# Kernel optimization log

Measured on AMD Instinct MI355X. Metric: run time of the kernel, lower is better.

Reference implementation:

```python
import jax, jax.numpy as jnp
import numpy as np

E = 1024      # hidden_size
H = 16        # num_attention_heads
HD = E // H   # head_dim
EPS = 1e-5


def _mw_linear(x, Wt, bt, Wi, bi, split):
    # multiway linear: text weights on tokens [:split], image weights on [split:]
    xt = x[:, :split] @ Wt.T + bt
    xi = x[:, split:] @ Wi.T + bi
    return jnp.concatenate([xt, xi], axis=1)


def _ln(x, g, b):
    mu = jnp.mean(x, axis=-1, keepdims=True)
    var = jnp.mean(jnp.square(x - mu), axis=-1, keepdims=True)
    return (x - mu) * jax.lax.rsqrt(var + EPS) * g + b


def _mw_ln(x, gt, bt, gi, bi, split):
    return jnp.concatenate([_ln(x[:, :split], gt, bt), _ln(x[:, split:], gi, bi)], axis=1)


def setup_inputs() -> dict:
    key = jax.random.key(0)
    ks = jax.random.split(key, 24)
    B, T = 8, 1024
    d = {
        'query': jax.random.normal(ks[0], (B, T, E), jnp.float32),
        'key': jax.random.normal(ks[1], (B, T, E), jnp.float32),
        'value': jax.random.normal(ks[2], (B, T, E), jnp.float32),
        'attention_mask': jax.random.normal(ks[3], (T, T), jnp.float32) * 0.02,
    }
    i = 4
    for name in ['q', 'k', 'v', 'o']:
        d[f'W{name}_t'] = jax.random.normal(ks[i], (E, E), jnp.float32) * 0.02; i += 1
        d[f'b{name}_t'] = jnp.zeros((E,), jnp.float32)
        d[f'W{name}_i'] = jax.random.normal(ks[i], (E, E), jnp.float32) * 0.02; i += 1
        d[f'b{name}_i'] = jnp.zeros((E,), jnp.float32)
    d['ln_g_t'] = jnp.ones((E,), jnp.float32)
    d['ln_b_t'] = jnp.zeros((E,), jnp.float32)
    d['ln_g_i'] = jnp.ones((E,), jnp.float32)
    d['ln_b_i'] = jnp.zeros((E,), jnp.float32)
    d['split_position'] = 64
    return d


def reference(query, key, value, attention_mask,
              Wq_t, bq_t, Wq_i, bq_i,
              Wk_t, bk_t, Wk_i, bk_i,
              Wv_t, bv_t, Wv_i, bv_i,
              Wo_t, bo_t, Wo_i, bo_i,
              ln_g_t, ln_b_t, ln_g_i, ln_b_i,
              split_position):
    B, T, _ = query.shape
    S = key.shape[1]
    scaling = HD ** -0.5
    q = _mw_linear(query, Wq_t, bq_t, Wq_i, bq_i, split_position) * scaling
    k = _mw_linear(key, Wk_t, bk_t, Wk_i, bk_i, split_position)
    v = _mw_linear(value, Wv_t, bv_t, Wv_i, bv_i, split_position)
    q = q.reshape(B, T, H, HD)
    k = k.reshape(B, S, H, HD)
    v = v.reshape(B, S, H, HD)
    # [B, H, T, S] attention logits
    attn_weights = jnp.einsum('bthd,bshd->bhts', q, k)
    attn_weights = jnp.nan_to_num(attn_weights) + attention_mask[None, None]
    probs = jax.nn.softmax(attn_weights.astype(jnp.float32), axis=-1).astype(attn_weights.dtype)
    attn = jnp.einsum('bhts,bshd->bthd', probs, v).reshape(B, T, E)
    attn = _mw_ln(attn, ln_g_t, ln_b_t, ln_g_i, ln_b_i, split_position)
    attn = _mw_linear(attn, Wo_t, bo_t, Wo_i, bo_i, split_position)
    return attn
```

## Files before the change

### kernel.cpp

```cpp
#include <hip/hip_runtime.h>

#define E_DIM 1024
#define HEADS 16
#define HD 64

typedef unsigned short ushort_t;
typedef __attribute__((ext_vector_type(8))) short bf16x8;
typedef __attribute__((ext_vector_type(4))) float floatx4;

__device__ inline unsigned int pack2bf(float a, float b) {
    unsigned int ua = __builtin_bit_cast(unsigned int, a);
    unsigned int ub = __builtin_bit_cast(unsigned int, b);
    ua = (ua + 0x8000u) >> 16;
    ub = (ub + 0x8000u) & 0xFFFF0000u;
    return ua | ub;
}
__device__ inline unsigned short f2bf(float a) {
    return (unsigned short)((__builtin_bit_cast(unsigned int, a) + 0x8000u) >> 16);
}
__device__ inline float bf2f(unsigned int s) {
    return __builtin_bit_cast(float, s << 16);
}

__device__ __forceinline__ void load_lds16(const void* g, void* l) {
    __builtin_amdgcn_global_load_lds(
        (const __attribute__((address_space(1))) unsigned int*)g,
        (__attribute__((address_space(3))) unsigned int*)l, 16, 0, 0);
}

__global__ __launch_bounds__(256) void cvt_inputs(
    const float* s0, const float* s1, const float* s2,
    ushort_t* d0, ushort_t* d1, ushort_t* d2)
{
    const float* __restrict__ src = (blockIdx.y == 0) ? s0 : (blockIdx.y == 1) ? s1 : s2;
    ushort_t* __restrict__ dst = (blockIdx.y == 0) ? d0 : (blockIdx.y == 1) ? d1 : d2;
    size_t i = ((size_t)blockIdx.x * 256 + threadIdx.x) * 8;
    float4 a = *(const float4*)&src[i];
    float4 b = *(const float4*)&src[i + 4];
    uint4 o;
    o.x = pack2bf(a.x, a.y); o.y = pack2bf(a.z, a.w);
    o.z = pack2bf(b.x, b.y); o.w = pack2bf(b.z, b.w);
    *(uint4*)&dst[i] = o;
}

__global__ __launch_bounds__(256) void cvt_weights(
    const float* w0, const float* w1, const float* w2, const float* w3,
    const float* w4, const float* w5, const float* w6, const float* w7,
    ushort_t* __restrict__ out)
{
    const float* srcs[8] = {w0, w1, w2, w3, w4, w5, w6, w7};
    const float* __restrict__ src = srcs[blockIdx.y];
    ushort_t* __restrict__ dst = out + (size_t)blockIdx.y * E_DIM * E_DIM;
    size_t i = ((size_t)blockIdx.x * 256 + threadIdx.x) * 8;
    float4 a = *(const float4*)&src[i];
    float4 b = *(const float4*)&src[i + 4];
    uint4 o;
    o.x = pack2bf(a.x, a.y); o.y = pack2bf(a.z, a.w);
    o.z = pack2bf(b.x, b.y); o.w = pack2bf(b.z, b.w);
    *(uint4*)&dst[i] = o;
}

template<bool OUT_BF16>
__device__ __forceinline__ void gemm_core(
    const ushort_t* __restrict__ x, const ushort_t* __restrict__ W,
    const float* __restrict__ bias, void* __restrict__ outv,
    int m0, int n0, int split, int kind, float scale, int T_)
{
    __shared__ __align__(16) ushort_t As[128 * 32];
    __shared__ __align__(16) ushort_t Bs[128 * 32];

    const int tid  = threadIdx.x;
    const int lane = tid & 63;
    const int wv   = tid >> 6;
    const int rw   = (wv >> 1) * 64;
    const int cw   = (wv & 1) * 64;
    const int am   = lane & 15;
    const int aq   = lane >> 4;

    const int grow = wv * 32 + (lane >> 2);
    const int gcol = (lane & 3) * 8;

    floatx4 acc[4][4];
    #pragma unroll
    for (int i = 0; i < 4; ++i)
        #pragma unroll
        for (int j = 0; j < 4; ++j)
            acc[i][j] = (floatx4){0.f, 0.f, 0.f, 0.f};

    for (int k0 = 0; k0 < E_DIM; k0 += 32) {
        load_lds16(&x[(size_t)(m0 + grow) * E_DIM + k0 + gcol],      &As[(wv * 32) * 32]);
        load_lds16(&x[(size_t)(m0 + grow + 16) * E_DIM + k0 + gcol], &As[(wv * 32 + 16) * 32]);
        load_lds16(&W[(size_t)(n0 + grow) * E_DIM + k0 + gcol],      &Bs[(wv * 32) * 32]);
        load_lds16(&W[(size_t)(n0 + grow + 16) * E_DIM + k0 + gcol], &Bs[(wv * 32 + 16) * 32]);
        __syncthreads();

        bf16x8 af[4], bfv[4];
        #pragma unroll
        for (int i = 0; i < 4; ++i)
            af[i] = *(const bf16x8*)&As[(rw + i * 16 + am) * 32 + aq * 8];
        #pragma unroll
        for (int j = 0; j < 4; ++j)
            bfv[j] = *(const bf16x8*)&Bs[(cw + j * 16 + am) * 32 + aq * 8];

        #pragma unroll
        for (int i = 0; i < 4; ++i)
            #pragma unroll
            for (int j = 0; j < 4; ++j)
                acc[i][j] = __builtin_amdgcn_mfma_f32_16x16x32_bf16(af[i], bfv[j], acc[i][j], 0, 0, 0);
        __syncthreads();
    }

    const int cq = lane >> 4;
    const int cm = lane & 15;
    #pragma unroll
    for (int j = 0; j < 4; ++j) {
        int n = n0 + cw + j * 16 + cm;
        float bv = bias[n];
        #pragma unroll
        for (int i = 0; i < 4; ++i) {
            int mbase = m0 + rw + i * 16 + cq * 4;
            #pragma unroll
            for (int r = 0; r < 4; ++r) {
                int m = mbase + r;
                int t = m % T_;
                if (((t < split) ? 0 : 1) != kind) continue;
                float val = (acc[i][j][r] + bv) * scale;
                if (OUT_BF16) ((ushort_t*)outv)[(size_t)m * E_DIM + n] = f2bf(val);
                else          ((float*)outv)[(size_t)m * E_DIM + n] = val;
            }
        }
    }
}

__global__ __launch_bounds__(256) void gemm_qkv(
    const ushort_t* __restrict__ xq, const ushort_t* __restrict__ xk,
    const ushort_t* __restrict__ xv, const ushort_t* __restrict__ wall,
    const float* bq_t, const float* bq_i, const float* bk_t, const float* bk_i,
    const float* bv_t, const float* bv_i,
    ushort_t* oq, ushort_t* ok, ushort_t* ov,
    const int* __restrict__ split_ptr, int T_)
{
    const int split = *split_ptr;
    const int z = blockIdx.z;
    const int op = z >> 1;
    const int kind = z & 1;
    const int m0 = blockIdx.y * 128;
    const int n0 = blockIdx.x * 128;
    const int t0 = m0 % T_;

    if (kind == 0) { if (t0 >= split) return; }
    else           { if (t0 + 128 <= split) return; }

    const ushort_t* x = (op == 0) ? xq : (op == 1) ? xk : xv;
    ushort_t* outp    = (op == 0) ? oq : (op == 1) ? ok : ov;
    const ushort_t* W = wall + (size_t)z * E_DIM * E_DIM;
    const float* bias = (op == 0) ? (kind ? bq_i : bq_t)
                      : (op == 1) ? (kind ? bk_i : bk_t)
                                  : (kind ? bv_i : bv_t);
    float scale = (op == 0) ? 0.125f : 1.0f;

    gemm_core<true>(x, W, bias, outp, m0, n0, split, kind, scale, T_);
}

__global__ __launch_bounds__(256) void gemm_o(
    const ushort_t* __restrict__ x, const ushort_t* __restrict__ Wt,
    const float* bt, const ushort_t* __restrict__ Wi, const float* bi,
    float* __restrict__ outp, const int* __restrict__ split_ptr, int T_)
{
    const int split = *split_ptr;
    const int kind = blockIdx.z;
    const int m0 = blockIdx.y * 128;
    const int n0 = blockIdx.x * 128;
    const int t0 = m0 % T_;

    if (kind == 0) { if (t0 >= split) return; }
    else           { if (t0 + 128 <= split) return; }

    gemm_core<false>(x, kind ? Wi : Wt, kind ? bi : bt, outp, m0, n0, split, kind, 1.0f, T_);
}

__global__ __launch_bounds__(256) void attn_mfma4(
    const ushort_t* __restrict__ q, const ushort_t* __restrict__ k,
    const ushort_t* __restrict__ v, const float* __restrict__ mask,
    ushort_t* __restrict__ outp, int T_)
{
    const int tid  = threadIdx.x;
    const int lane = tid & 63;
    const int wv   = tid >> 6;
    const int h    = blockIdx.y;
    const int b    = blockIdx.z;
    const int r0   = blockIdx.x * 128;

    __shared__ __align__(16) unsigned short Ks[2 * 5120];
    __shared__ __align__(16) unsigned short Vst[2 * 5120];
    __shared__ __align__(16) unsigned short Ps[4 * 1280];

    const int m    = lane & 15;
    const int kq   = lane >> 4;
    const int wrow = wv * 16;

    bf16x8 aq[2][2];
    #pragma unroll
    for (int qs = 0; qs < 2; ++qs)
        #pragma unroll
        for (int c = 0; c < 2; ++c)
            aq[qs][c] = *(const bf16x8*)&q[((size_t)(b * T_ + r0 + qs * 64 + wrow + m)) * E_DIM
                                           + h * HD + c * 32 + kq * 8];

    floatx4 oa[2][4];
    float mrun[2][4], lsum[2][4];
    #pragma unroll
    for (int qs = 0; qs < 2; ++qs)
        #pragma unroll
        for (int j = 0; j < 4; ++j) {
            oa[qs][j] = (floatx4){0.f, 0.f, 0.f, 0.f};
            mrun[qs][j] = -3.0e38f; lsum[qs][j] = 0.f;
        }

    const int krow = tid >> 4;
    const int kc4  = (tid & 15) * 4;
    const int kad  = (kc4 >> 5) * 2560 + krow * 40 + (kc4 & 31);
    const int vs0  = (tid >> 4) * 4;
    const int vd0  = (tid & 15) * 4;
    const int vplane = (vs0 >> 5) * 2560;
    const int vsin   = vs0 & 31;

    uint2 kreg[4], vreg[4];

    #pragma unroll
    for (int i = 0; i < 4; ++i)
        kreg[i] = *(const uint2*)&k[((size_t)(b * T_ + krow + 16 * i)) * E_DIM + h * HD + kc4];
    #pragma unroll
    for (int i = 0; i < 4; ++i)
        vreg[i] = *(const uint2*)&v[((size_t)(b * T_ + vs0 + i)) * E_DIM + h * HD + vd0];

    #pragma unroll
    for (int i = 0; i < 4; ++i) {
        int ad = kad + 16 * i * 40;
        *(unsigned int*)&Ks[ad]     = kreg[i].x;
        *(unsigned int*)&Ks[ad + 2] = kreg[i].y;
    }
    {
        const ushort_t* vp = (const ushort_t*)vreg;
        #pragma unroll
        for (int t = 0; t < 4; ++t) {
            int d  = vd0 + t;
            int pr = d ^ ((d >> 4) & 3);
            uint2 w;
            w.x = (unsigned int)vp[0 * 4 + t] | ((unsigned int)vp[1 * 4 + t] << 16);
            w.y = (unsigned int)vp[2 * 4 + t] | ((unsigned int)vp[3 * 4 + t] << 16);
            *(uint2*)&Vst[vplane + pr * 40 + vsin] = w;
        }
    }
    __syncthreads();

    const int NT = T_ / 64;
    #pragma unroll 1
    for (int it = 0; it < NT; ++it) {
        const int cur = (it & 1) * 5120;
        const int nxt = ((it + 1) & 1) * 5120;
        const int s0 = it * 64;

        if (it + 1 < NT) {
            int s0n = s0 + 64;
            #pragma unroll
            for (int i = 0; i < 4; ++i)
                kreg[i] = *(const uint2*)&k[((size_t)(b * T_ + s0n + krow + 16 * i)) * E_DIM + h * HD + kc4];
            #pragma unroll
            for (int i = 0; i < 4; ++i)
                vreg[i] = *(const uint2*)&v[((size_t)(b * T_ + s0n + vs0 + i)) * E_DIM + h * HD + vd0];
        }

        #pragma unroll
        for (int qs = 0; qs < 2; ++qs) {
            float mv[4][4];
            {
                const float* mbase = &mask[(size_t)(r0 + qs * 64 + wrow + kq * 4) * T_ + s0 + m];
                #pragma unroll
                for (int j = 0; j < 4; ++j)
                    #pragma unroll
                    for (int r = 0; r < 4; ++r)
                        mv[j][r] = mbase[r * T_ + j * 16];
            }

            floatx4 sa[4];
            #pragma unroll
            for (int j = 0; j < 4; ++j) sa[j] = (floatx4){0.f, 0.f, 0.f, 0.f};
            #pragma unroll
            for (int c = 0; c < 2; ++c) {
                #pragma unroll
                for (int j = 0; j < 4; ++j) {
                    bf16x8 bk = *(const bf16x8*)&Ks[cur + c * 2560 + (j * 16 + m) * 40 + kq * 8];
                    sa[j] = __builtin_amdgcn_mfma_f32_16x16x32_bf16(aq[qs][c], bk, sa[j], 0, 0, 0);
                }
            }

            float mnew[4], alpha[4];
            #pragma unroll
            for (int r = 0; r < 4; ++r) {
                sa[0][r] += mv[0][r]; sa[1][r] += mv[1][r];
                sa[2][r] += mv[2][r]; sa[3][r] += mv[3][r];
                float mt = fmaxf(fmaxf(sa[0][r], sa[1][r]), fmaxf(sa[2][r], sa[3][r]));
                mt = fmaxf(mt, __shfl_xor(mt, 1));
                mt = fmaxf(mt, __shfl_xor(mt, 2));
                mt = fmaxf(mt, __shfl_xor(mt, 4));
                mt = fmaxf(mt, __shfl_xor(mt, 8));
                float mn = fmaxf(mrun[qs][r], mt);
                alpha[r] = __expf(mrun[qs][r] - mn);
                mnew[r] = mn;
                mrun[qs][r] = mn;
            }
            #pragma unroll
            for (int j = 0; j < 4; ++j)
                #pragma unroll
                for (int r = 0; r < 4; ++r)
                    oa[qs][j][r] *= alpha[r];

            float rs[4] = {0.f, 0.f, 0.f, 0.f};
            #pragma unroll
            for (int j = 0; j < 4; ++j) {
                int gl = ((((j & 1) << 1) | (m >> 3)) ^ kq) & 3;
                int pbase = wv * 1280 + (j >> 1) * 640 + (kq * 4) * 40 + gl * 8 + (m & 7);
                #pragma unroll
                for (int r = 0; r < 4; ++r) {
                    float p = __expf(sa[j][r] - mnew[r]);
                    rs[r] += p;
                    Ps[pbase + r * 40] = f2bf(p);
                }
            }
            #pragma unroll
            for (int r = 0; r < 4; ++r) {
                float s = rs[r];
                s += __shfl_xor(s, 1); s += __shfl_xor(s, 2);
                s += __shfl_xor(s, 4); s += __shfl_xor(s, 8);
                lsum[qs][r] = lsum[qs][r] * alpha[r] + s;
            }

            #pragma unroll
            for (int c = 0; c < 2; ++c) {
                bf16x8 ap = *(const bf16x8*)&Ps[wv * 1280 + c * 640 + m * 40 + ((kq ^ (m >> 2)) & 3) * 8];
                #pragma unroll
                for (int j = 0; j < 4; ++j) {
                    int pr = 16 * j + (m ^ j);
                    bf16x8 bv = *(const bf16x8*)&Vst[cur + c * 2560 + pr * 40 + kq * 8];
                    oa[qs][j] = __builtin_amdgcn_mfma_f32_16x16x32_bf16(ap, bv, oa[qs][j], 0, 0, 0);
                }
            }
        }

        if (it + 1 < NT) {
            #pragma unroll
            for (int i = 0; i < 4; ++i) {
                int ad = nxt + kad + 16 * i * 40;
                *(unsigned int*)&Ks[ad]     = kreg[i].x;
                *(unsigned int*)&Ks[ad + 2] = kreg[i].y;
            }
            const ushort_t* vp = (const ushort_t*)vreg;
            #pragma unroll
            for (int t = 0; t < 4; ++t) {
                int d  = vd0 + t;
                int pr = d ^ ((d >> 4) & 3);
                uint2 w;
                w.x = (unsigned int)vp[0 * 4 + t] | ((unsigned int)vp[1 * 4 + t] << 16);
                w.y = (unsigned int)vp[2 * 4 + t] | ((unsigned int)vp[3 * 4 + t] << 16);
                *(uint2*)&Vst[nxt + vplane + pr * 40 + vsin] = w;
            }
            __syncthreads();
        }
    }

    #pragma unroll
    for (int qs = 0; qs < 2; ++qs)
        #pragma unroll
        for (int r = 0; r < 4; ++r) {
            float inv = 1.0f / lsum[qs][r];
            size_t orow = ((size_t)(b * T_ + r0 + qs * 64 + wrow + kq * 4 + r)) * E_DIM + h * HD;
            #pragma unroll
            for (int j = 0; j < 4; ++j)
                outp[orow + j * 16 + m] = f2bf(oa[qs][j][r] * inv);
        }
}

__global__ __launch_bounds__(256) void mw_ln_bf16(
    const ushort_t* __restrict__ x,
    const float* __restrict__ gt, const float* __restrict__ bt,
    const float* __restrict__ gi, const float* __restrict__ bi,
    ushort_t* __restrict__ out,
    const int* __restrict__ split_ptr, int T_)
{
    const int split = *split_ptr;
    const int row = blockIdx.x;
    const int t = row % T_;
    const float* __restrict__ g  = (t < split) ? gt : gi;
    const float* __restrict__ bb = (t < split) ? bt : bi;

    const int tid = threadIdx.x;
    const int lane = tid & 63;
    const int wid = tid >> 6;

    __shared__ float red[8];

    uint2 xv = *(const uint2*)&x[(size_t)row * E_DIM + tid * 4];
    float f0 = bf2f(xv.x & 0xffffu), f1 = bf2f(xv.x >> 16);
    float f2 = bf2f(xv.y & 0xffffu), f3 = bf2f(xv.y >> 16);
    float s = f0 + f1 + f2 + f3;
    #pragma unroll
    for (int off = 1; off < 64; off <<= 1) s += __shfl_xor(s, off, 64);
    if (lane == 0) red[wid] = s;
    __syncthreads();
    float mu = (red[0] + red[1] + red[2] + red[3]) * (1.0f / E_DIM);

    float d0 = f0 - mu, d1 = f1 - mu, d2 = f2 - mu, d3 = f3 - mu;
    float s2 = d0*d0 + d1*d1 + d2*d2 + d3*d3;
    #pragma unroll
    for (int off = 1; off < 64; off <<= 1) s2 += __shfl_xor(s2, off, 64);
    if (lane == 0) red[4 + wid] = s2;
    __syncthreads();
    float var = (red[4] + red[5] + red[6] + red[7]) * (1.0f / E_DIM);
    float rstd = rsqrtf(var + 1e-5f);

    float4 gv = *(const float4*)&g[tid * 4];
    float4 bv = *(const float4*)&bb[tid * 4];
    uint2 ov;
    ov.x = pack2bf(d0 * rstd * gv.x + bv.x, d1 * rstd * gv.y + bv.y);
    ov.y = pack2bf(d2 * rstd * gv.z + bv.z, d3 * rstd * gv.w + bv.w);
    *(uint2*)&out[(size_t)row * E_DIM + tid * 4] = ov;
}

extern "C" void kernel_launch(void* const* d_in, const int* in_sizes, int n_in,
                              void* d_out, int out_size, void* d_ws, size_t ws_size,
                              hipStream_t stream) {
    const float* query = (const float*)d_in[0];
    const float* key   = (const float*)d_in[1];
    const float* value = (const float*)d_in[2];
    const float* mask  = (const float*)d_in[3];
    const float* Wq_t = (const float*)d_in[4];  const float* bq_t = (const float*)d_in[5];
    const float* Wq_i = (const float*)d_in[6];  const float* bq_i = (const float*)d_in[7];
    const float* Wk_t = (const float*)d_in[8];  const float* bk_t = (const float*)d_in[9];
    const float* Wk_i = (const float*)d_in[10]; const float* bk_i = (const float*)d_in[11];
    const float* Wv_t = (const float*)d_in[12]; const float* bv_t = (const float*)d_in[13];
    const float* Wv_i = (const float*)d_in[14]; const float* bv_i = (const float*)d_in[15];
    const float* Wo_t = (const float*)d_in[16]; const float* bo_t = (const float*)d_in[17];
    const float* Wo_i = (const float*)d_in[18]; const float* bo_i = (const float*)d_in[19];
    const float* ln_g_t = (const float*)d_in[20]; const float* ln_b_t = (const float*)d_in[21];
    const float* ln_g_i = (const float*)d_in[22]; const float* ln_b_i = (const float*)d_in[23];
    const int* split = (const int*)d_in[24];

    float* out = (float*)d_out;

    const int BT = in_sizes[0] / E_DIM;
    const int T_ = 1024;
    const int B  = BT / T_;

    ushort_t* ws = (ushort_t*)d_ws;
    const size_t nx = (size_t)BT * E_DIM;
    const size_t nw = (size_t)E_DIM * E_DIM;
    ushort_t* xq_bf = ws;
    ushort_t* xk_bf = ws + nx;
    ushort_t* xv_bf = ws + 2 * nx;
    ushort_t* k_bf  = ws + 3 * nx;
    ushort_t* v_bf  = ws + 4 * nx;
    ushort_t* w_bf  = ws + 5 * nx;
    ushort_t* q_bf  = (ushort_t*)d_out;

    dim3 blk(256);
    const int cvt_blocks = (int)(nx / 2048);
    const int wcvt_blocks = (int)(nw / 2048);

    cvt_weights<<<dim3(wcvt_blocks, 8), blk, 0, stream>>>(
        Wq_t, Wq_i, Wk_t, Wk_i, Wv_t, Wv_i, Wo_t, Wo_i, w_bf);
    cvt_inputs<<<dim3(cvt_blocks, 3), blk, 0, stream>>>(
        query, key, value, xq_bf, xk_bf, xv_bf);

    gemm_qkv<<<dim3(E_DIM / 128, BT / 128, 6), blk, 0, stream>>>(
        xq_bf, xk_bf, xv_bf, w_bf,
        bq_t, bq_i, bk_t, bk_i, bv_t, bv_i,
        q_bf, k_bf, v_bf, split, T_);

    attn_mfma4<<<dim3(T_ / 128, HEADS, B), blk, 0, stream>>>(
        q_bf, k_bf, v_bf, mask, q_bf, T_);

    mw_ln_bf16<<<dim3(BT), blk, 0, stream>>>(
        q_bf, ln_g_t, ln_b_t, ln_g_i, ln_b_i, xq_bf, split, T_);

    gemm_o<<<dim3(E_DIM / 128, BT / 128, 2), blk, 0, stream>>>(
        xq_bf, w_bf + 6 * nw, bo_t, w_bf + 7 * nw, bo_i, out, split, T_);
}
```

Measured before the change: 496.3 us.

## Single-buffer attention K/V LDS, lazy softmax rescale, MFMA priority, reorder grid

```diff
diff --git a/kernel.cpp b/kernel.cpp
--- a/kernel.cpp
+++ b/kernel.cpp
@@ -187,12 +187,12 @@
     const int tid  = threadIdx.x;
     const int lane = tid & 63;
     const int wv   = tid >> 6;
+    const int b    = blockIdx.x;
     const int h    = blockIdx.y;
-    const int b    = blockIdx.z;
-    const int r0   = blockIdx.x * 128;
-
-    __shared__ __align__(16) unsigned short Ks[2 * 5120];
-    __shared__ __align__(16) unsigned short Vst[2 * 5120];
+    const int r0   = blockIdx.z * 128;
+
+    __shared__ __align__(16) unsigned short Ks[5120];
+    __shared__ __align__(16) unsigned short Vst[5120];
     __shared__ __align__(16) unsigned short Ps[4 * 1280];
 
     const int m    = lane & 15;
@@ -257,8 +257,6 @@
     const int NT = T_ / 64;
     #pragma unroll 1
     for (int it = 0; it < NT; ++it) {
-        const int cur = (it & 1) * 5120;
-        const int nxt = ((it + 1) & 1) * 5120;
         const int s0 = it * 64;
 
         if (it + 1 < NT) {
@@ -286,35 +284,43 @@
             floatx4 sa[4];
             #pragma unroll
             for (int j = 0; j < 4; ++j) sa[j] = (floatx4){0.f, 0.f, 0.f, 0.f};
+            __builtin_amdgcn_s_setprio(1);
             #pragma unroll
             for (int c = 0; c < 2; ++c) {
                 #pragma unroll
                 for (int j = 0; j < 4; ++j) {
-                    bf16x8 bk = *(const bf16x8*)&Ks[cur + c * 2560 + (j * 16 + m) * 40 + kq * 8];
+                    bf16x8 bk = *(const bf16x8*)&Ks[c * 2560 + (j * 16 + m) * 40 + kq * 8];
                     sa[j] = __builtin_amdgcn_mfma_f32_16x16x32_bf16(aq[qs][c], bk, sa[j], 0, 0, 0);
                 }
             }
-
-            float mnew[4], alpha[4];
+            __builtin_amdgcn_s_setprio(0);
+
+            float mt[4];
             #pragma unroll
             for (int r = 0; r < 4; ++r) {
                 sa[0][r] += mv[0][r]; sa[1][r] += mv[1][r];
                 sa[2][r] += mv[2][r]; sa[3][r] += mv[3][r];
-                float mt = fmaxf(fmaxf(sa[0][r], sa[1][r]), fmaxf(sa[2][r], sa[3][r]));
-                mt = fmaxf(mt, __shfl_xor(mt, 1));
-                mt = fmaxf(mt, __shfl_xor(mt, 2));
-                mt = fmaxf(mt, __shfl_xor(mt, 4));
-                mt = fmaxf(mt, __shfl_xor(mt, 8));
-                float mn = fmaxf(mrun[qs][r], mt);
-                alpha[r] = __expf(mrun[qs][r] - mn);
-                mnew[r] = mn;
-                mrun[qs][r] = mn;
-            }
-            #pragma unroll
-            for (int j = 0; j < 4; ++j)
+                float m2 = fmaxf(fmaxf(sa[0][r], sa[1][r]), fmaxf(sa[2][r], sa[3][r]));
+                m2 = fmaxf(m2, __shfl_xor(m2, 1));
+                m2 = fmaxf(m2, __shfl_xor(m2, 2));
+                m2 = fmaxf(m2, __shfl_xor(m2, 4));
+                m2 = fmaxf(m2, __shfl_xor(m2, 8));
+                mt[r] = m2;
+            }
+            float need = fmaxf(fmaxf(mt[0] - mrun[qs][0], mt[1] - mrun[qs][1]),
+                               fmaxf(mt[2] - mrun[qs][2], mt[3] - mrun[qs][3]));
+            if (!__all(need <= 8.0f)) {
                 #pragma unroll
-                for (int r = 0; r < 4; ++r)
-                    oa[qs][j][r] *= alpha[r];
+                for (int r = 0; r < 4; ++r) {
+                    float mn = fmaxf(mrun[qs][r], mt[r]);
+                    float a  = __expf(mrun[qs][r] - mn);
+                    mrun[qs][r] = mn;
+                    lsum[qs][r] *= a;
+                    #pragma unroll
+                    for (int j = 0; j < 4; ++j)
+                        oa[qs][j][r] *= a;
+                }
+            }
 
             float rs[4] = {0.f, 0.f, 0.f, 0.f};
             #pragma unroll
@@ -323,7 +329,7 @@
                 int pbase = wv * 1280 + (j >> 1) * 640 + (kq * 4) * 40 + gl * 8 + (m & 7);
                 #pragma unroll
                 for (int r = 0; r < 4; ++r) {
-                    float p = __expf(sa[j][r] - mnew[r]);
+                    float p = __expf(sa[j][r] - mrun[qs][r]);
                     rs[r] += p;
                     Ps[pbase + r * 40] = f2bf(p);
                 }
@@ -333,25 +339,28 @@
                 float s = rs[r];
                 s += __shfl_xor(s, 1); s += __shfl_xor(s, 2);
                 s += __shfl_xor(s, 4); s += __shfl_xor(s, 8);
-                lsum[qs][r] = lsum[qs][r] * alpha[r] + s;
-            }
-
+                lsum[qs][r] += s;
+            }
+
+            __builtin_amdgcn_s_setprio(1);
             #pragma unroll
             for (int c = 0; c < 2; ++c) {
                 bf16x8 ap = *(const bf16x8*)&Ps[wv * 1280 + c * 640 + m * 40 + ((kq ^ (m >> 2)) & 3) * 8];
                 #pragma unroll
                 for (int j = 0; j < 4; ++j) {
                     int pr = 16 * j + (m ^ j);
-                    bf16x8 bv = *(const bf16x8*)&Vst[cur + c * 2560 + pr * 40 + kq * 8];
+                    bf16x8 bv = *(const bf16x8*)&Vst[c * 2560 + pr * 40 + kq * 8];
                     oa[qs][j] = __builtin_amdgcn_mfma_f32_16x16x32_bf16(ap, bv, oa[qs][j], 0, 0, 0);
                 }
             }
+            __builtin_amdgcn_s_setprio(0);
         }
 
         if (it + 1 < NT) {
+            __syncthreads();
             #pragma unroll
             for (int i = 0; i < 4; ++i) {
-                int ad = nxt + kad + 16 * i * 40;
+                int ad = kad + 16 * i * 40;
                 *(unsigned int*)&Ks[ad]     = kreg[i].x;
                 *(unsigned int*)&Ks[ad + 2] = kreg[i].y;
             }
@@ -363,7 +372,7 @@
                 uint2 w;
                 w.x = (unsigned int)vp[0 * 4 + t] | ((unsigned int)vp[1 * 4 + t] << 16);
                 w.y = (unsigned int)vp[2 * 4 + t] | ((unsigned int)vp[3 * 4 + t] << 16);
-                *(uint2*)&Vst[nxt + vplane + pr * 40 + vsin] = w;
+                *(uint2*)&Vst[vplane + pr * 40 + vsin] = w;
             }
             __syncthreads();
         }
@@ -477,7 +486,7 @@
         bq_t, bq_i, bk_t, bk_i, bv_t, bv_i,
         q_bf, k_bf, v_bf, split, T_);
 
-    attn_mfma4<<<dim3(T_ / 128, HEADS, B), blk, 0, stream>>>(
+    attn_mfma4<<<dim3(B, HEADS, T_ / 128), blk, 0, stream>>>(
         q_bf, k_bf, v_bf, mask, q_bf, T_);
 
     mw_ln_bf16<<<dim3(BT), blk, 0, stream>>>(
```

After: 498.2 us. About the same (+0.4%).
